# Optimization experiments

Hardware: AMD Instinct MI355X
Metric: run time of the kernel (lower is better)

The kernel has to match this reference:

```python
import math
import jax, jax.numpy as jnp
import numpy as np

T, D, H = 2048, 1024, 16
DH = D // H
DFF = 4 * D
EPS = 1e-5


def gelu(x):
    c = math.sqrt(2.0 / math.pi)
    return 0.5 * x * (1.0 + jnp.tanh(c * (x + 0.044715 * jnp.power(x, 3))))


def layer_norm(x, w, b):
    mu = jnp.mean(x, axis=-1, keepdims=True)
    var = jnp.var(x, axis=-1, keepdims=True)
    return (x - mu) / jnp.sqrt(var + EPS) * w + b


def setup_inputs() -> dict:
    key = jax.random.key(0)
    ks = jax.random.split(key, 8)
    s = lambda fan_in: 1.0 / math.sqrt(fan_in)
    return {
        "x": jax.random.normal(ks[0], (T, D), jnp.float32),
        "w_kqv": jax.random.uniform(ks[1], (3 * D, D), jnp.float32, -s(D), s(D)),
        "b_kqv": jnp.zeros((3 * D,), jnp.float32),
        "w_o": jax.random.uniform(ks[2], (D, D), jnp.float32, -s(D), s(D)),
        "b_o": jnp.zeros((D,), jnp.float32),
        "ln1_w": jnp.ones((D,), jnp.float32),
        "ln1_b": jnp.zeros((D,), jnp.float32),
        "ln2_w": jnp.ones((D,), jnp.float32),
        "ln2_b": jnp.zeros((D,), jnp.float32),
        "w_up": jax.random.uniform(ks[3], (DFF, D), jnp.float32, -s(D), s(D)),
        "b_up": jnp.zeros((DFF,), jnp.float32),
        "w_down": jax.random.uniform(ks[4], (D, DFF), jnp.float32, -s(DFF), s(DFF)),
        "b_down": jnp.zeros((D,), jnp.float32),
    }


def _block(x, w_kqv, b_kqv, w_o, b_o, ln1_w, ln1_b, ln2_w, ln2_b,
           w_up, b_up, w_down, b_down):
    t = x.shape[0]
    # --- causal attention ---
    h = layer_norm(x, ln1_w, ln1_b)
    kqv = h @ w_kqv.T + b_kqv                      # [t, 3D]
    k, q, v = jnp.split(kqv, 3, axis=-1)
    # rearrange 't (d h) -> h t d' : head index is the FAST axis (as in source)
    to_heads = lambda m: m.reshape(t, DH, H).transpose(2, 0, 1)  # [H, t, DH]
    k, q, v = to_heads(k), to_heads(q), to_heads(v)
    # NOTE: source divides by sqrt(1/d) == multiplies by sqrt(d_head)
    logits = jnp.einsum('hqd,hkd->hqk', q, k) * math.sqrt(DH)
    mask = jnp.tril(jnp.ones((t, t), dtype=bool))
    logits = jnp.where(mask, logits, -jnp.inf)
    attn_w = jax.nn.softmax(logits, axis=-1)       # [H, t, t]
    hv = jnp.einsum('hqK,hKd->hqd', attn_w, v)     # [H, t, DH]
    # rearrange 'h q d -> q (h d)' : head index is the SLOW axis (as in source)
    hv = hv.transpose(1, 0, 2).reshape(t, D)
    x = x + (hv @ w_o.T + b_o)
    # --- MLP ---
    h2 = layer_norm(x, ln2_w, ln2_b)
    z = gelu(h2 @ w_up.T + b_up) @ w_down.T + b_down
    return x + z


def reference(x, w_kqv, b_kqv, w_o, b_o, ln1_w, ln1_b, ln2_w, ln2_b,
              w_up, b_up, w_down, b_down):
    return _block(x, w_kqv, b_kqv, w_o, b_o, ln1_w, ln1_b, ln2_w, ln2_b,
                  w_up, b_up, w_down, b_down)
```

## Files before the change

kernel.cpp:

```cpp
#include <hip/hip_runtime.h>
#include <math.h>

#define TT 2048
#define DD 1024
#define NH 16
#define DHD 64
#define DFF 4096

typedef __attribute__((ext_vector_type(8))) short short8;
typedef __attribute__((ext_vector_type(4))) float f32x4;

#define MFMA16(a, b, c) __builtin_amdgcn_mfma_f32_16x16x32_bf16(a, b, c, 0, 0, 0)
#define GLDS16(gp, lp) __builtin_amdgcn_global_load_lds( \
    (const __attribute__((address_space(1))) void*)(gp), \
    (__attribute__((address_space(3))) void*)(lp), 16, 0, 0)

static __device__ __forceinline__ unsigned short f2b(float f) {
  unsigned u = __builtin_bit_cast(unsigned, f);
  u = u + 0x7fffu + ((u >> 16) & 1u);
  return (unsigned short)(u >> 16);
}
static __device__ __forceinline__ float b2f(unsigned short b) {
  return __builtin_bit_cast(float, (unsigned)b << 16);
}

__global__ __launch_bounds__(256) void f2b4_kernel(const float* __restrict__ s0,
    const float* __restrict__ s1, const float* __restrict__ s2,
    const float* __restrict__ s3, unsigned short* __restrict__ out) {
  int i = blockIdx.x * 256 + threadIdx.x;
  const float* s; int off;
  if (i < 786432)       { s = s0; off = 0; }
  else if (i < 1048576) { s = s1; off = 786432; }
  else if (i < 2097152) { s = s2; off = 1048576; }
  else                  { s = s3; off = 2097152; }
  float4 v = ((const float4*)s)[i - off];
  ushort4 o;
  o.x = f2b(v.x); o.y = f2b(v.y); o.z = f2b(v.z); o.w = f2b(v.w);
  ((ushort4*)out)[i] = o;
}

__global__ __launch_bounds__(256) void ln_kernel(const float* __restrict__ x,
    const float* __restrict__ w, const float* __restrict__ b,
    unsigned short* __restrict__ out) {
  int row = blockIdx.x;
  const float4* xr = (const float4*)(x + (size_t)row * DD);
  float4 v = xr[threadIdx.x];
  float s  = v.x + v.y + v.z + v.w;
  float ss = v.x * v.x + v.y * v.y + v.z * v.z + v.w * v.w;
  for (int o = 32; o > 0; o >>= 1) {
    s  += __shfl_down(s, o);
    ss += __shfl_down(ss, o);
  }
  __shared__ float red[10];
  int lane = threadIdx.x & 63, wv = threadIdx.x >> 6;
  if (lane == 0) { red[wv] = s; red[4 + wv] = ss; }
  __syncthreads();
  if (threadIdx.x == 0) {
    float S  = red[0] + red[1] + red[2] + red[3];
    float SS = red[4] + red[5] + red[6] + red[7];
    float mu  = S * (1.0f / DD);
    float var = SS * (1.0f / DD) - mu * mu;
    red[8] = mu;
    red[9] = rsqrtf(var + 1e-5f);
  }
  __syncthreads();
  float mu = red[8], inv = red[9];
  float4 wv4 = ((const float4*)w)[threadIdx.x];
  float4 bv4 = ((const float4*)b)[threadIdx.x];
  ushort4 o4;
  o4.x = f2b((v.x - mu) * inv * wv4.x + bv4.x);
  o4.y = f2b((v.y - mu) * inv * wv4.y + bv4.y);
  o4.z = f2b((v.z - mu) * inv * wv4.z + bv4.z);
  o4.w = f2b((v.w - mu) * inv * wv4.w + bv4.w);
  ((ushort4*)(out + (size_t)row * DD))[threadIdx.x] = o4;
}

template<int FUSE_GELU, int OUT_BF16, int HAS_RESID, int PARTIAL>
__global__ __launch_bounds__(256) void gemm4(
    const unsigned short* __restrict__ A,
    const unsigned short* __restrict__ Bw,
    const float* __restrict__ bias,
    const float* __restrict__ resid,
    void* __restrict__ Cout,
    int M, int N, int K, int KS, int CX, int CY) {
  __shared__ char lds[65536];
  const int tid = threadIdx.x;
  const int w = tid >> 6, l = tid & 63;
  const int l15 = l & 15, lhi = l >> 4;

  const int GX = N >> 7, GYM = M >> 7;
  const int xcd = blockIdx.x & 7, s = blockIdx.x >> 3;
  const int ncx = GX / CX;
  const int bx = (xcd % ncx) * CX + (s % CX);
  const int yz = (xcd / ncx) * CY + (s / CX);
  const int by = yz % GYM, bz = yz / GYM;

  const int row0 = by << 7, col0 = bx << 7;
  const int kbeg = bz * KS;
  const int wm = (w >> 1) * 64, wn = (w & 1) * 64;

  f32x4 acc[4][4] = {};

  const int lr = l >> 3;
  const int cb = ((l & 7) * 16) ^ (lr << 4);
  const char* aS = (const char*)A + ((size_t)(row0 + w * 32 + lr) * K + kbeg) * 2 + cb;
  const char* bS = (const char*)Bw + ((size_t)(col0 + w * 32 + lr) * K + kbeg) * 2 + cb;
  const size_t r8 = (size_t)K * 16;
  const int aO = w * 4096, bO = 16384 + w * 4096;
  const int NT = KS >> 6;

  auto STAGE = [&](int t) {
    char* base = lds + (t & 1) * 32768;
    const char* a = aS + (size_t)t * 128;
    const char* b = bS + (size_t)t * 128;
    GLDS16(a,            base + aO);
    GLDS16(a +     r8,   base + aO + 1024);
    GLDS16(a + 2 * r8,   base + aO + 2048);
    GLDS16(a + 3 * r8,   base + aO + 3072);
    GLDS16(b,            base + bO);
    GLDS16(b +     r8,   base + bO + 1024);
    GLDS16(b + 2 * r8,   base + bO + 2048);
    GLDS16(b + 3 * r8,   base + bO + 3072);
  };
  auto COMPUTE = [&](int t) {
    const char* Ab = lds + (t & 1) * 32768;
    const char* Bb = Ab + 16384;
    const int sw = (l15 & 7) << 4;
#pragma unroll
    for (int kk = 0; kk < 2; ++kk) {
      short8 af[4], bf[4];
#pragma unroll
      for (int mi = 0; mi < 4; ++mi)
        af[mi] = *(const short8*)(Ab + (wm + mi * 16 + l15) * 128 + ((kk * 64 + lhi * 16) ^ sw));
#pragma unroll
      for (int ni = 0; ni < 4; ++ni)
        bf[ni] = *(const short8*)(Bb + (wn + ni * 16 + l15) * 128 + ((kk * 64 + lhi * 16) ^ sw));
#pragma unroll
      for (int mi = 0; mi < 4; ++mi)
#pragma unroll
        for (int ni = 0; ni < 4; ++ni)
          acc[mi][ni] = MFMA16(af[mi], bf[ni], acc[mi][ni]);
    }
  };

  STAGE(0);
  for (int t = 0; t < NT; ++t) {
    if (t + 1 < NT) STAGE(t + 1);
    __builtin_amdgcn_sched_barrier(0);
    if (t + 1 < NT) asm volatile("s_waitcnt vmcnt(8)" ::: "memory");
    else            asm volatile("s_waitcnt vmcnt(0)" ::: "memory");
    __builtin_amdgcn_s_barrier();
    __builtin_amdgcn_sched_barrier(0);
    COMPUTE(t);
    __builtin_amdgcn_sched_barrier(0);
    __builtin_amdgcn_s_barrier();
  }

  if (PARTIAL) {
    unsigned short* Cp = (unsigned short*)Cout + (size_t)bz * M * N;
#pragma unroll
    for (int mi = 0; mi < 4; ++mi)
#pragma unroll
      for (int r = 0; r < 4; ++r) {
        size_t row = (size_t)(row0 + wm + mi * 16 + lhi * 4 + r);
#pragma unroll
        for (int ni = 0; ni < 4; ++ni)
          Cp[row * N + col0 + wn + ni * 16 + l15] = f2b(acc[mi][ni][r]);
      }
    return;
  }

#pragma unroll
  for (int mi = 0; mi < 4; ++mi) {
#pragma unroll
    for (int r = 0; r < 4; ++r) {
      size_t row = (size_t)(row0 + wm + mi * 16 + lhi * 4 + r);
#pragma unroll
      for (int ni = 0; ni < 4; ++ni) {
        int col = col0 + wn + ni * 16 + l15;
        float v = acc[mi][ni][r] + bias[col];
        if (FUSE_GELU) {
          float u = v;
          v = 0.5f * u * (1.0f + tanhf(0.7978845608028654f * (u + 0.044715f * u * u * u)));
        }
        if (HAS_RESID) v += resid[row * N + col];
        if (OUT_BF16) ((unsigned short*)Cout)[row * N + col] = f2b(v);
        else          ((float*)Cout)[row * N + col] = v;
      }
    }
  }
}

template<int NP>
__global__ __launch_bounds__(256) void reduce_k(const unsigned short* __restrict__ p,
    const float* __restrict__ bias, const float* __restrict__ resid,
    float* __restrict__ out) {
  int i = blockIdx.x * 256 + threadIdx.x;
  float4 r = ((const float4*)resid)[i];
  float4 bb = ((const float4*)bias)[i & (DD / 4 - 1)];
  float o0 = r.x + bb.x, o1 = r.y + bb.y, o2 = r.z + bb.z, o3 = r.w + bb.w;
#pragma unroll
  for (int z = 0; z < NP; ++z) {
    ushort4 pv = ((const ushort4*)(p + (size_t)z * TT * DD))[i];
    o0 += b2f(pv.x); o1 += b2f(pv.y); o2 += b2f(pv.z); o3 += b2f(pv.w);
  }
  float4 o; o.x = o0; o.y = o1; o.z = o2; o.w = o3;
  ((float4*)out)[i] = o;
}

__global__ __launch_bounds__(256) void gather_qkv(const unsigned short* __restrict__ kqv,
    unsigned short* __restrict__ Q, unsigned short* __restrict__ K) {
  int idx = blockIdx.x * 256 + threadIdx.x;
  int d = idx & 63;
  int t = (idx >> 6) & (TT - 1);
  int h = idx >> 17;
  int col = d * NH + h;
  const unsigned short* rowp = kqv + (size_t)t * (3 * DD);
  K[idx] = rowp[col];
  Q[idx] = f2b(b2f(rowp[DD + col]) * 8.0f);
}

__global__ __launch_bounds__(256) void transpose_v(const unsigned short* __restrict__ kqv,
    unsigned short* __restrict__ Vt) {
  const int h = blockIdx.y;
  const int t0 = blockIdx.x * 64;
  __shared__ unsigned short Vs[64][65];
  for (int idx = threadIdx.x; idx < 4096; idx += 256) {
    int t = idx >> 6, d = idx & 63;
    Vs[t][d] = kqv[(size_t)(t0 + t) * (3 * DD) + 2 * DD + d * NH + h];
  }
  __syncthreads();
  for (int idx = threadIdx.x; idx < 4096; idx += 256) {
    int d = idx >> 6, t = idx & 63;
    Vt[(size_t)(h * DHD + d) * TT + t0 + t] = Vs[t][d];
  }
}

__global__ __launch_bounds__(256) void attn_mfma(
    const unsigned short* __restrict__ Q,
    const unsigned short* __restrict__ K,
    const unsigned short* __restrict__ Vt,
    unsigned short* __restrict__ hv) {
  const int bid = blockIdx.x;
  const int xcd = bid & 7, s = bid >> 3;
  const int qb = 31 - (s & 31);
  const int h  = xcd * 2 + (s >> 5);
  const int q0 = qb * 64;
  const int tid = threadIdx.x;
  const int w = tid >> 6, l = tid & 63;
  const int l15 = l & 15, lhi = l >> 4;

  __shared__ char lds[40960];
  char* Ps = lds + 32768 + w * 2048;

  const char* KhB = (const char*)(K + (size_t)h * TT * DHD);
  const char* VhB = (const char*)(Vt + (size_t)h * DHD * TT);

  const unsigned short* Qbase = Q + ((size_t)h * TT + q0 + w * 16 + l15) * DHD;
  short8 qf0 = *(const short8*)(Qbase + lhi * 8);
  short8 qf1 = *(const short8*)(Qbase + 32 + lhi * 8);

  f32x4 oacc[4] = {};
  float m = -1e30f, lsum = 0.0f;

  const int lr = l >> 3;
  const int colb = ((l & 7) * 16) ^ (lr << 4);
  const int srow = w * 16 + lr;
  const int swz = (l15 & 7) << 4;

  auto stage = [&](int k0n, char* buf) {
    const char* ks = KhB + (size_t)(k0n + srow) * 128 + colb;
    GLDS16(ks, buf + w * 2048);
    GLDS16(ks + 8 * 128, buf + w * 2048 + 1024);
    const char* vs = VhB + (size_t)srow * (TT * 2) + (size_t)k0n * 2 + colb;
    GLDS16(vs, buf + 8192 + w * 2048);
    GLDS16(vs + 8 * (TT * 2), buf + 8192 + w * 2048 + 1024);
  };

  stage(0, lds);
  int cur = 0;

  for (int kt = 0; kt <= qb; ++kt) {
    if (kt < qb) stage((kt + 1) * 64, lds + (cur ^ 1) * 16384);
    __builtin_amdgcn_sched_barrier(0);
    if (kt < qb) asm volatile("s_waitcnt vmcnt(4)" ::: "memory");
    else         asm volatile("s_waitcnt vmcnt(0)" ::: "memory");
    __builtin_amdgcn_s_barrier();
    __builtin_amdgcn_sched_barrier(0);

    const char* Kb = lds + cur * 16384;
    const char* Vb = Kb + 8192;

    f32x4 sacc[4] = {};
    __builtin_amdgcn_s_setprio(1);
#pragma unroll
    for (int nt = 0; nt < 4; ++nt) {
      const char* rp = Kb + (nt * 16 + l15) * 128;
      short8 kb0 = *(const short8*)(rp + ((lhi * 16) ^ swz));
      short8 kb1 = *(const short8*)(rp + ((64 + lhi * 16) ^ swz));
      sacc[nt] = MFMA16(kb0, qf0, sacc[nt]);
      sacc[nt] = MFMA16(kb1, qf1, sacc[nt]);
    }
    __builtin_amdgcn_s_setprio(0);

    if (kt == qb) {
      const int qloc = w * 16 + l15;
#pragma unroll
      for (int nt = 0; nt < 4; ++nt)
#pragma unroll
        for (int r = 0; r < 4; ++r)
          if (nt * 16 + lhi * 4 + r > qloc) sacc[nt][r] = -1e30f;
    }

    float tmax = -1e30f;
#pragma unroll
    for (int nt = 0; nt < 4; ++nt)
#pragma unroll
      for (int r = 0; r < 4; ++r) tmax = fmaxf(tmax, sacc[nt][r]);
    tmax = fmaxf(tmax, __shfl_xor(tmax, 16));
    tmax = fmaxf(tmax, __shfl_xor(tmax, 32));
    float mnew = fmaxf(m, tmax);
    float al = __expf(m - mnew);
    m = mnew;
    float ssum = 0.0f;
#pragma unroll
    for (int nt = 0; nt < 4; ++nt)
#pragma unroll
      for (int r = 0; r < 4; ++r) {
        float p = __expf(sacc[nt][r] - mnew);
        sacc[nt][r] = p;
        ssum += p;
      }
    ssum += __shfl_xor(ssum, 16);
    ssum += __shfl_xor(ssum, 32);
    lsum = lsum * al + ssum;

    {
      char* pp = Ps + l15 * 128;
#pragma unroll
      for (int nt = 0; nt < 4; ++nt) {
        uint2 pk;
        pk.x = (unsigned)f2b(sacc[nt][0]) | ((unsigned)f2b(sacc[nt][1]) << 16);
        pk.y = (unsigned)f2b(sacc[nt][2]) | ((unsigned)f2b(sacc[nt][3]) << 16);
        *(uint2*)(pp + (((nt * 16 + lhi * 4) * 2) ^ swz)) = pk;
      }
    }

    float alr[4];
#pragma unroll
    for (int r = 0; r < 4; ++r) alr[r] = __shfl(al, (l & 48) | (lhi * 4 + r));
#pragma unroll
    for (int dt = 0; dt < 4; ++dt)
#pragma unroll
      for (int r = 0; r < 4; ++r) oacc[dt][r] *= alr[r];

    const char* pr = Ps + l15 * 128;
    short8 pa0 = *(const short8*)(pr + ((lhi * 16) ^ swz));
    short8 pa1 = *(const short8*)(pr + ((64 + lhi * 16) ^ swz));
    __builtin_amdgcn_s_setprio(1);
#pragma unroll
    for (int dt = 0; dt < 4; ++dt) {
      const char* vr = Vb + (dt * 16 + l15) * 128;
      short8 vb0 = *(const short8*)(vr + ((lhi * 16) ^ swz));
      short8 vb1 = *(const short8*)(vr + ((64 + lhi * 16) ^ swz));
      oacc[dt] = MFMA16(pa0, vb0, oacc[dt]);
      oacc[dt] = MFMA16(pa1, vb1, oacc[dt]);
    }
    __builtin_amdgcn_s_setprio(0);

    __builtin_amdgcn_sched_barrier(0);
    __builtin_amdgcn_s_barrier();
    cur ^= 1;
  }

  float lr4[4];
#pragma unroll
  for (int r = 0; r < 4; ++r)
    lr4[r] = 1.0f / __shfl(lsum, (l & 48) | (lhi * 4 + r));
#pragma unroll
  for (int r = 0; r < 4; ++r) {
    size_t orow = (size_t)(q0 + w * 16 + lhi * 4 + r) * DD + h * 64;
#pragma unroll
    for (int dt = 0; dt < 4; ++dt)
      hv[orow + dt * 16 + l15] = f2b(oacc[dt][r] * lr4[r]);
  }
}

extern "C" void kernel_launch(void* const* d_in, const int* in_sizes, int n_in,
                              void* d_out, int out_size, void* d_ws, size_t ws_size,
                              hipStream_t stream) {
  const float* x     = (const float*)d_in[0];
  const float* w_kqv = (const float*)d_in[1];
  const float* b_kqv = (const float*)d_in[2];
  const float* w_o   = (const float*)d_in[3];
  const float* b_o   = (const float*)d_in[4];
  const float* ln1_w = (const float*)d_in[5];
  const float* ln1_b = (const float*)d_in[6];
  const float* ln2_w = (const float*)d_in[7];
  const float* ln2_b = (const float*)d_in[8];
  const float* w_up  = (const float*)d_in[9];
  const float* b_up  = (const float*)d_in[10];
  const float* w_dn  = (const float*)d_in[11];
  const float* b_dn  = (const float*)d_in[12];
  float* out = (float*)d_out;

  char* W = (char*)d_ws;
  unsigned short* wkqv_b = (unsigned short*)(W);
  unsigned short* wo_b   = (unsigned short*)(W + 6291456);
  unsigned short* wup_b  = (unsigned short*)(W + 8388608);
  unsigned short* wdn_b  = (unsigned short*)(W + 16777216);
  unsigned short* h_b    = (unsigned short*)(W + 25165824);
  unsigned short* kqz    = (unsigned short*)(W + 29360128);
  unsigned short* Qg     = (unsigned short*)(W + 46137344);
  unsigned short* Kg     = (unsigned short*)(W + 50331648);
  unsigned short* Vtg    = (unsigned short*)(W + 54525952);
  unsigned short* hv_b   = (unsigned short*)(W + 58720256);
  float*          x2     = (float*)(W + 62914560);
  unsigned short* pproj  = (unsigned short*)(W + 29360128);
  unsigned short* pdown  = (unsigned short*)(W + 46137344);

  f2b4_kernel<<<3145728 / 256, 256, 0, stream>>>(w_kqv, w_o, w_up, w_dn, wkqv_b);

  ln_kernel<<<TT, 256, 0, stream>>>(x, ln1_w, ln1_b, h_b);
  gemm4<0, 1, 0, 0><<<384, 256, 0, stream>>>(
      h_b, wkqv_b, b_kqv, nullptr, kqz, TT, 3 * DD, DD, DD, 6, 8);
  gather_qkv<<<(NH * TT * DHD) / 256, 256, 0, stream>>>(kqz, Qg, Kg);
  transpose_v<<<dim3(TT / 64, NH), 256, 0, stream>>>(kqz, Vtg);
  attn_mfma<<<512, 256, 0, stream>>>(Qg, Kg, Vtg, hv_b);
  gemm4<0, 0, 0, 1><<<256, 256, 0, stream>>>(
      hv_b, wo_b, nullptr, nullptr, pproj, TT, DD, DD, DD / 2, 8, 4);
  reduce_k<2><<<TT * DD / 4 / 256, 256, 0, stream>>>(pproj, b_o, x, x2);
  ln_kernel<<<TT, 256, 0, stream>>>(x2, ln2_w, ln2_b, h_b);
  gemm4<1, 1, 0, 0><<<512, 256, 0, stream>>>(
      h_b, wup_b, b_up, nullptr, kqz, TT, DFF, DD, DD, 8, 8);
  gemm4<0, 0, 0, 1><<<512, 256, 0, stream>>>(
      kqz, wdn_b, nullptr, nullptr, pdown, TT, DD, DFF, DFF / 4, 8, 8);
  reduce_k<4><<<TT * DD / 4 / 256, 256, 0, stream>>>(pdown, b_dn, x2, out);
}
```

Baseline: 171.4 us.

## Switch GEMMs to split-K with BK=32 tiles and separate bias/GELU reduce kernels

```diff
diff --git a/kernel.cpp b/kernel.cpp
--- a/kernel.cpp
+++ b/kernel.cpp
@@ -75,15 +75,13 @@
   ((ushort4*)(out + (size_t)row * DD))[threadIdx.x] = o4;
 }
 
-template<int FUSE_GELU, int OUT_BF16, int HAS_RESID, int PARTIAL>
-__global__ __launch_bounds__(256) void gemm4(
+__global__ __launch_bounds__(256, 4) void gemm6(
     const unsigned short* __restrict__ A,
     const unsigned short* __restrict__ Bw,
-    const float* __restrict__ bias,
-    const float* __restrict__ resid,
-    void* __restrict__ Cout,
-    int M, int N, int K, int KS, int CX, int CY) {
-  __shared__ char lds[65536];
+    unsigned short* __restrict__ Cp,
+    unsigned short* __restrict__ Cp2,
+    int M, int N, int K, int KS, int CX, int CY, int SPLITA) {
+  __shared__ char lds[32768];
   const int tid = threadIdx.x;
   const int w = tid >> 6, l = tid & 63;
   const int l15 = l & 15, lhi = l >> 4;
@@ -101,53 +99,47 @@
 
   f32x4 acc[4][4] = {};
 
-  const int lr = l >> 3;
-  const int cb = ((l & 7) * 16) ^ (lr << 4);
-  const char* aS = (const char*)A + ((size_t)(row0 + w * 32 + lr) * K + kbeg) * 2 + cb;
-  const char* bS = (const char*)Bw + ((size_t)(col0 + w * 32 + lr) * K + kbeg) * 2 + cb;
-  const size_t r8 = (size_t)K * 16;
-  const int aO = w * 4096, bO = 16384 + w * 4096;
-  const int NT = KS >> 6;
+  const int srow = w * 32 + (l >> 2);
+  const int scol = (l & 3) * 16;
+  const char* aS = (const char*)A + ((size_t)(row0 + srow) * K + kbeg) * 2 + scol;
+  const char* bS = (const char*)Bw + ((size_t)(col0 + srow) * K + kbeg) * 2 + scol;
+  const size_t r16 = (size_t)K * 32;
+  const int aO = w * 2048, bO = 8192 + w * 2048;
+  const int NT = KS >> 5;
 
   auto STAGE = [&](int t) {
-    char* base = lds + (t & 1) * 32768;
-    const char* a = aS + (size_t)t * 128;
-    const char* b = bS + (size_t)t * 128;
-    GLDS16(a,            base + aO);
-    GLDS16(a +     r8,   base + aO + 1024);
-    GLDS16(a + 2 * r8,   base + aO + 2048);
-    GLDS16(a + 3 * r8,   base + aO + 3072);
-    GLDS16(b,            base + bO);
-    GLDS16(b +     r8,   base + bO + 1024);
-    GLDS16(b + 2 * r8,   base + bO + 2048);
-    GLDS16(b + 3 * r8,   base + bO + 3072);
+    char* base = lds + (t & 1) * 16384;
+    const char* a = aS + (size_t)t * 64;
+    const char* b = bS + (size_t)t * 64;
+    GLDS16(a,       base + aO);
+    GLDS16(a + r16, base + aO + 1024);
+    GLDS16(b,       base + bO);
+    GLDS16(b + r16, base + bO + 1024);
   };
   auto COMPUTE = [&](int t) {
-    const char* Ab = lds + (t & 1) * 32768;
-    const char* Bb = Ab + 16384;
-    const int sw = (l15 & 7) << 4;
-#pragma unroll
-    for (int kk = 0; kk < 2; ++kk) {
-      short8 af[4], bf[4];
-#pragma unroll
-      for (int mi = 0; mi < 4; ++mi)
-        af[mi] = *(const short8*)(Ab + (wm + mi * 16 + l15) * 128 + ((kk * 64 + lhi * 16) ^ sw));
+    const char* Ab = lds + (t & 1) * 16384;
+    const char* Bb = Ab + 8192;
+    short8 af[4], bf[4];
+#pragma unroll
+    for (int mi = 0; mi < 4; ++mi)
+      af[mi] = *(const short8*)(Ab + (wm + mi * 16 + l15) * 64 + lhi * 16);
+#pragma unroll
+    for (int ni = 0; ni < 4; ++ni)
+      bf[ni] = *(const short8*)(Bb + (wn + ni * 16 + l15) * 64 + lhi * 16);
+    __builtin_amdgcn_s_setprio(1);
+#pragma unroll
+    for (int mi = 0; mi < 4; ++mi)
 #pragma unroll
       for (int ni = 0; ni < 4; ++ni)
-        bf[ni] = *(const short8*)(Bb + (wn + ni * 16 + l15) * 128 + ((kk * 64 + lhi * 16) ^ sw));
-#pragma unroll
-      for (int mi = 0; mi < 4; ++mi)
-#pragma unroll
-        for (int ni = 0; ni < 4; ++ni)
-          acc[mi][ni] = MFMA16(af[mi], bf[ni], acc[mi][ni]);
-    }
+        acc[mi][ni] = MFMA16(af[mi], bf[ni], acc[mi][ni]);
+    __builtin_amdgcn_s_setprio(0);
   };
 
   STAGE(0);
   for (int t = 0; t < NT; ++t) {
     if (t + 1 < NT) STAGE(t + 1);
     __builtin_amdgcn_sched_barrier(0);
-    if (t + 1 < NT) asm volatile("s_waitcnt vmcnt(8)" ::: "memory");
+    if (t + 1 < NT) asm volatile("s_waitcnt vmcnt(4)" ::: "memory");
     else            asm volatile("s_waitcnt vmcnt(0)" ::: "memory");
     __builtin_amdgcn_s_barrier();
     __builtin_amdgcn_sched_barrier(0);
@@ -156,39 +148,43 @@
     __builtin_amdgcn_s_barrier();
   }
 
-  if (PARTIAL) {
-    unsigned short* Cp = (unsigned short*)Cout + (size_t)bz * M * N;
-#pragma unroll
-    for (int mi = 0; mi < 4; ++mi)
-#pragma unroll
-      for (int r = 0; r < 4; ++r) {
-        size_t row = (size_t)(row0 + wm + mi * 16 + lhi * 4 + r);
-#pragma unroll
-        for (int ni = 0; ni < 4; ++ni)
-          Cp[row * N + col0 + wn + ni * 16 + l15] = f2b(acc[mi][ni][r]);
-      }
-    return;
-  }
-
-#pragma unroll
-  for (int mi = 0; mi < 4; ++mi) {
+  unsigned short* base;
+  size_t off;
+  if (bz < SPLITA) { base = Cp;  off = (size_t)bz * M * N; }
+  else             { base = Cp2; off = (size_t)(bz - SPLITA) * M * N; }
+#pragma unroll
+  for (int mi = 0; mi < 4; ++mi)
 #pragma unroll
     for (int r = 0; r < 4; ++r) {
       size_t row = (size_t)(row0 + wm + mi * 16 + lhi * 4 + r);
 #pragma unroll
-      for (int ni = 0; ni < 4; ++ni) {
-        int col = col0 + wn + ni * 16 + l15;
-        float v = acc[mi][ni][r] + bias[col];
-        if (FUSE_GELU) {
-          float u = v;
-          v = 0.5f * u * (1.0f + tanhf(0.7978845608028654f * (u + 0.044715f * u * u * u)));
-        }
-        if (HAS_RESID) v += resid[row * N + col];
-        if (OUT_BF16) ((unsigned short*)Cout)[row * N + col] = f2b(v);
-        else          ((float*)Cout)[row * N + col] = v;
-      }
+      for (int ni = 0; ni < 4; ++ni)
+        base[off + row * N + col0 + wn + ni * 16 + l15] = f2b(acc[mi][ni][r]);
     }
-  }
+}
+
+template<int GELU>
+__global__ __launch_bounds__(256) void reduce2b(const unsigned short* __restrict__ p0,
+    const unsigned short* __restrict__ p1, const float* __restrict__ bias,
+    unsigned short* __restrict__ out, int n4) {
+  int i = blockIdx.x * 256 + threadIdx.x;
+  ushort4 a = ((const ushort4*)p0)[i];
+  ushort4 b = ((const ushort4*)p1)[i];
+  float4 bb = ((const float4*)bias)[i % n4];
+  float v0 = b2f(a.x) + b2f(b.x) + bb.x;
+  float v1 = b2f(a.y) + b2f(b.y) + bb.y;
+  float v2 = b2f(a.z) + b2f(b.z) + bb.z;
+  float v3 = b2f(a.w) + b2f(b.w) + bb.w;
+  if (GELU) {
+    const float c = 0.7978845608028654f;
+    v0 = 0.5f * v0 * (1.0f + tanhf(c * (v0 + 0.044715f * v0 * v0 * v0)));
+    v1 = 0.5f * v1 * (1.0f + tanhf(c * (v1 + 0.044715f * v1 * v1 * v1)));
+    v2 = 0.5f * v2 * (1.0f + tanhf(c * (v2 + 0.044715f * v2 * v2 * v2)));
+    v3 = 0.5f * v3 * (1.0f + tanhf(c * (v3 + 0.044715f * v3 * v3 * v3)));
+  }
+  ushort4 o;
+  o.x = f2b(v0); o.y = f2b(v1); o.z = f2b(v2); o.w = f2b(v3);
+  ((ushort4*)out)[i] = o;
 }
 
 template<int NP>
@@ -203,6 +199,24 @@
   for (int z = 0; z < NP; ++z) {
     ushort4 pv = ((const ushort4*)(p + (size_t)z * TT * DD))[i];
     o0 += b2f(pv.x); o1 += b2f(pv.y); o2 += b2f(pv.z); o3 += b2f(pv.w);
+  }
+  float4 o; o.x = o0; o.y = o1; o.z = o2; o.w = o3;
+  ((float4*)out)[i] = o;
+}
+
+__global__ __launch_bounds__(256) void reduce8(const unsigned short* __restrict__ pA,
+    const unsigned short* __restrict__ pB, const float* __restrict__ bias,
+    const float* __restrict__ resid, float* __restrict__ out) {
+  int i = blockIdx.x * 256 + threadIdx.x;
+  float4 r = ((const float4*)resid)[i];
+  float4 bb = ((const float4*)bias)[i & (DD / 4 - 1)];
+  float o0 = r.x + bb.x, o1 = r.y + bb.y, o2 = r.z + bb.z, o3 = r.w + bb.w;
+#pragma unroll
+  for (int z = 0; z < 4; ++z) {
+    ushort4 pv = ((const ushort4*)(pA + (size_t)z * TT * DD))[i];
+    o0 += b2f(pv.x); o1 += b2f(pv.y); o2 += b2f(pv.z); o3 += b2f(pv.w);
+    ushort4 qv = ((const ushort4*)(pB + (size_t)z * TT * DD))[i];
+    o0 += b2f(qv.x); o1 += b2f(qv.y); o2 += b2f(qv.z); o3 += b2f(qv.w);
   }
   float4 o; o.x = o0; o.y = o1; o.z = o2; o.w = o3;
   ((float4*)out)[i] = o;
@@ -410,30 +424,34 @@
   unsigned short* wup_b  = (unsigned short*)(W + 8388608);
   unsigned short* wdn_b  = (unsigned short*)(W + 16777216);
   unsigned short* h_b    = (unsigned short*)(W + 25165824);
-  unsigned short* kqz    = (unsigned short*)(W + 29360128);
+  unsigned short* rA     = (unsigned short*)(W + 29360128);
+  unsigned short* rB     = (unsigned short*)(W + 46137344);
   unsigned short* Qg     = (unsigned short*)(W + 46137344);
   unsigned short* Kg     = (unsigned short*)(W + 50331648);
   unsigned short* Vtg    = (unsigned short*)(W + 54525952);
   unsigned short* hv_b   = (unsigned short*)(W + 58720256);
   float*          x2     = (float*)(W + 62914560);
-  unsigned short* pproj  = (unsigned short*)(W + 29360128);
-  unsigned short* pdown  = (unsigned short*)(W + 46137344);
+  unsigned short* pB2    = (unsigned short*)(W);
 
   f2b4_kernel<<<3145728 / 256, 256, 0, stream>>>(w_kqv, w_o, w_up, w_dn, wkqv_b);
 
   ln_kernel<<<TT, 256, 0, stream>>>(x, ln1_w, ln1_b, h_b);
-  gemm4<0, 1, 0, 0><<<384, 256, 0, stream>>>(
-      h_b, wkqv_b, b_kqv, nullptr, kqz, TT, 3 * DD, DD, DD, 6, 8);
-  gather_qkv<<<(NH * TT * DHD) / 256, 256, 0, stream>>>(kqz, Qg, Kg);
-  transpose_v<<<dim3(TT / 64, NH), 256, 0, stream>>>(kqz, Vtg);
+  gemm6<<<768, 256, 0, stream>>>(h_b, wkqv_b, rA, rB,
+      TT, 3 * DD, DD, DD / 2, 3, 32, 1);
+  reduce2b<0><<<TT * 3 * DD / 4 / 256, 256, 0, stream>>>(
+      rA, rB, b_kqv, rA, 3 * DD / 4);
+  gather_qkv<<<(NH * TT * DHD) / 256, 256, 0, stream>>>(rA, Qg, Kg);
+  transpose_v<<<dim3(TT / 64, NH), 256, 0, stream>>>(rA, Vtg);
   attn_mfma<<<512, 256, 0, stream>>>(Qg, Kg, Vtg, hv_b);
-  gemm4<0, 0, 0, 1><<<256, 256, 0, stream>>>(
-      hv_b, wo_b, nullptr, nullptr, pproj, TT, DD, DD, DD / 2, 8, 4);
-  reduce_k<2><<<TT * DD / 4 / 256, 256, 0, stream>>>(pproj, b_o, x, x2);
+  gemm6<<<512, 256, 0, stream>>>(hv_b, wo_b, rA, rA,
+      TT, DD, DD, DD / 4, 1, 64, 4);
+  reduce_k<4><<<TT * DD / 4 / 256, 256, 0, stream>>>(rA, b_o, x, x2);
   ln_kernel<<<TT, 256, 0, stream>>>(x2, ln2_w, ln2_b, h_b);
-  gemm4<1, 1, 0, 0><<<512, 256, 0, stream>>>(
-      h_b, wup_b, b_up, nullptr, kqz, TT, DFF, DD, DD, 8, 8);
-  gemm4<0, 0, 0, 1><<<512, 256, 0, stream>>>(
-      kqz, wdn_b, nullptr, nullptr, pdown, TT, DD, DFF, DFF / 4, 8, 8);
-  reduce_k<4><<<TT * DD / 4 / 256, 256, 0, stream>>>(pdown, b_dn, x2, out);
-}
+  gemm6<<<1024, 256, 0, stream>>>(h_b, wup_b, rA, rB,
+      TT, DFF, DD, DD / 2, 4, 32, 1);
+  reduce2b<1><<<TT * DFF / 4 / 256, 256, 0, stream>>>(
+      rA, rB, b_up, rA, DFF / 4);
+  gemm6<<<1024, 256, 0, stream>>>(rA, wdn_b, rB, pB2,
+      TT, DD, DFF, DFF / 8, 1, 128, 4);
+  reduce8<<<TT * DD / 4 / 256, 256, 0, stream>>>(rB, pB2, b_dn, x2, out);
+}
```

Measured after the change: 212.3 us. 23.8% more time.
